# Performance work log

Hardware: AMD Instinct MI355X
Metric: run time of the kernel (lower is better)

## Reference

```python
import jax, jax.numpy as jnp
import numpy as np

COS_EPS = 1e-8  # torch F.cosine_similarity eps


def setup_inputs() -> dict:
    key = jax.random.key(0)
    k1, k2 = jax.random.split(key)
    x = jax.random.normal(k1, (8192, 512), dtype=jnp.float32)
    class_logits = jax.random.normal(k2, (8192, 100), dtype=jnp.float32)
    return {"x": x, "class_logits": class_logits}


def reference(x, class_logits):
    N, D = x.shape
    C = class_logits.shape[1]

    # class_logits.clone().detach()
    logits = jax.lax.stop_gradient(class_logits)
    pred = jax.nn.softmax(logits, axis=1)
    max_logit = pred.max(axis=1)          # [N]
    max_cls = pred.argmax(axis=1)         # [N] int

    # graph(): pairwise cosine similarity = normalize rows + gram matmul
    norms = jnp.linalg.norm(x, axis=1, keepdims=True)
    xn = x / jnp.maximum(norms, COS_EPS)
    mat = xn @ xn.T                       # [N, N]

    x_agg = mat @ x + x                   # [N, D]
    x_new = jax.lax.stop_gradient(x_agg)

    # update_prototype: per-class weighted scatter-add then mean over counts
    weighted = x_new * max_logit[:, None]                     # [N, D]
    sums = jax.ops.segment_sum(weighted, max_cls, num_segments=C)      # [C, D]
    counts = jax.ops.segment_sum(jnp.ones((N,), x.dtype), max_cls, num_segments=C)  # [C]
    prototypes = jnp.where(counts[:, None] > 0,
                           sums / jnp.maximum(counts, 1.0)[:, None],
                           jnp.zeros_like(sums))              # [C, D]

    # inter_class_matrix[i, j] = prototypes[j] - prototypes[i]
    inter_class_matrix = prototypes[None, :, :] - prototypes[:, None, :]  # [C, C, D]
    return prototypes, inter_class_matrix
```

## Files before the change

kernel.cpp:

```cpp
#include <hip/hip_runtime.h>
#include <math.h>

#define N_ROWS 8192
#define D_DIM  512
#define C_CLS  100

typedef unsigned short u16;
typedef unsigned int u32;
typedef __attribute__((ext_vector_type(8))) _Float16 half8;
typedef __attribute__((ext_vector_type(4))) float floatx4;

#define WS_G      0
#define WS_GP     262144
#define WS_INV    5505024
#define WS_WV     5513216
#define WS_CLS    5521408
#define WS_CNT    5529600
#define WS_OFFS   5529728
#define WS_ORDER  5529856
#define WS_U      5538048
#define WS_V      5589248
#define WS_ZTH    5640448

#define LDA 517

typedef const __attribute__((address_space(1))) u32* gp32;
typedef __attribute__((address_space(3))) u32* lp32;
__device__ __forceinline__ void cp16(const u16* g, u16* l) {
    __builtin_amdgcn_global_load_lds((gp32)g, (lp32)l, 16, 0, 0);
}

__device__ __forceinline__ u16 f2h(float v) {
    _Float16 h = (_Float16)v;
    return *(u16*)&h;
}

__global__ __launch_bounds__(256) void kA(const float* __restrict__ logits,
        const float* __restrict__ x, float* __restrict__ wv, int* __restrict__ cls,
        float* __restrict__ inv, u16* __restrict__ zth) {
    __shared__ float xs[16 * LDA];
    __shared__ float ns[4][16];
    __shared__ float sv_s[16];
    int bx = blockIdx.x, t = threadIdx.x;
    if (bx < 1024) {
        int lane = t & 63;
        int row0 = (bx << 3) + ((t >> 6) << 1);
        #pragma unroll
        for (int rr = 0; rr < 2; ++rr) {
            int row = row0 + rr;
            const float* lrow = logits + (size_t)row * C_CLS;
            float v1 = lrow[lane];
            bool has2 = (lane + 64) < C_CLS;
            float v2 = has2 ? lrow[lane + 64] : -INFINITY;
            float m; int idx;
            if (v2 > v1) { m = v2; idx = lane + 64; } else { m = v1; idx = lane; }
            #pragma unroll
            for (int off = 32; off >= 1; off >>= 1) {
                float om = __shfl_down(m, off);
                int   oi = __shfl_down(idx, off);
                if (om > m || (om == m && oi < idx)) { m = om; idx = oi; }
            }
            m = __shfl(m, 0);
            idx = __shfl(idx, 0);
            float s = expf(v1 - m) + (has2 ? expf(v2 - m) : 0.0f);
            #pragma unroll
            for (int off = 32; off >= 1; off >>= 1) s += __shfl_down(s, off);
            if (lane == 0) {
                wv[row] = 1.0f / s;
                cls[row] = idx;
            }
        }
        return;
    }
    int r0 = (bx - 1024) << 4;
    const float* src = x + (size_t)r0 * D_DIM;
    #pragma unroll
    for (int i = 0; i < 8; ++i) {
        int e = i * 1024 + t * 4;
        int r = e >> 9, c = e & 511;
        *(float4*)&xs[r * LDA + c] = *(const float4*)&src[e];
    }
    __syncthreads();
    {
        int r = t & 15, seg = t >> 4;
        const float* row = &xs[r * LDA + seg * 32];
        float ss = 0.f;
        #pragma unroll
        for (int jj = 0; jj < 32; ++jj) { float v = row[jj]; ss += v * v; }
        atomicAdd(&ns[seg & 3][r], 0.f);
        ns[0][r] = 0.f;
        __syncthreads();
        atomicAdd(&ns[0][r], ss);
    }
    __syncthreads();
    if (t < 16) {
        float iv = 1.0f / fmaxf(sqrtf(ns[0][t]), 1e-8f);
        inv[r0 + t] = iv;
        sv_s[t] = sqrtf(iv);
    }
    __syncthreads();
    int c = t >> 1, rq = (t & 1) * 8;
    float svl[8];
    #pragma unroll
    for (int ii = 0; ii < 8; ++ii) svl[ii] = sv_s[rq + ii];
    #pragma unroll
    for (int ct = 0; ct < 4; ++ct) {
        int d = ct * 128 + c;
        u16 o[8];
        #pragma unroll
        for (int ii = 0; ii < 8; ++ii)
            o[ii] = f2h(xs[(rq + ii) * LDA + d] * svl[ii]);
        uint4 val = make_uint4((u32)o[0] | ((u32)o[1] << 16),
                               (u32)o[2] | ((u32)o[3] << 16),
                               (u32)o[4] | ((u32)o[5] << 16),
                               (u32)o[6] | ((u32)o[7] << 16));
        *(uint4*)&zth[(size_t)d * N_ROWS + r0 + rq] = val;
    }
}

__global__ __launch_bounds__(1024) void kB(const int* __restrict__ cls,
        int* __restrict__ cnt, int* __restrict__ offs, int* __restrict__ order) {
    __shared__ int hist[128], scan_s[128], cur[128];
    int t = threadIdx.x;
    if (t < 128) hist[t] = 0;
    __syncthreads();
    for (int m = t; m < N_ROWS; m += 1024) atomicAdd(&hist[cls[m]], 1);
    __syncthreads();
    if (t < 128) scan_s[t] = hist[t];
    __syncthreads();
    #pragma unroll
    for (int d = 1; d < 128; d <<= 1) {
        int add = (t < 128 && t >= d) ? scan_s[t - d] : 0;
        __syncthreads();
        if (t < 128) scan_s[t] += add;
        __syncthreads();
    }
    if (t < 128) {
        int off0 = scan_s[t] - hist[t];
        cur[t] = off0;
        offs[t] = off0;
        cnt[t] = hist[t];
    }
    __syncthreads();
    for (int m = t; m < N_ROWS; m += 1024) {
        int p = atomicAdd(&cur[cls[m]], 1);
        order[p] = m;
    }
}

__global__ __launch_bounds__(256) void kC(const u16* __restrict__ zth,
        const float* __restrict__ x, const float* __restrict__ inv,
        const float* __restrict__ wv, const int* __restrict__ order,
        const int* __restrict__ offs, const int* __restrict__ cnt,
        float* __restrict__ Gp, float* __restrict__ u_arr, float* __restrict__ v_arr) {
    __shared__ __attribute__((aligned(16))) union {
        struct { u16 Ah[2][128 * 32], Bh[2][128 * 32]; } g;
        struct { float us[4][64], vs[4][64]; } uv;
    } sm;
    int bx = blockIdx.x, t = threadIdx.x;
    if (bx >= 320) {
        int idx = bx - 320;
        int c = idx >> 3, jc = idx & 7;
        int g = t >> 6, lane = t & 63;
        int j = jc * 64 + lane;
        int n = cnt[c], o = offs[c];
        float ua = 0.f, va = 0.f;
        for (int p = g; p < n; p += 4) {
            int m = order[o + p];
            float wm = wv[m];
            float wi = wm * inv[m];
            float xv = x[(size_t)m * D_DIM + j];
            ua += wi * xv; va += wm * xv;
        }
        sm.uv.us[g][lane] = ua; sm.uv.vs[g][lane] = va;
        __syncthreads();
        if (g == 0) {
            u_arr[(size_t)c * D_DIM + j] = sm.uv.us[0][lane] + sm.uv.us[1][lane] + sm.uv.us[2][lane] + sm.uv.us[3][lane];
            v_arr[(size_t)c * D_DIM + j] = sm.uv.vs[0][lane] + sm.uv.vs[1][lane] + sm.uv.vs[2][lane] + sm.uv.vs[3][lane];
        }
        return;
    }
    int tile = bx % 10;
    int p = bx / 10;
    int ti = tile < 4 ? 0 : (tile < 7 ? 1 : (tile < 9 ? 2 : 3));
    int tj = tile - (ti == 0 ? 0 : (ti == 1 ? 3 : (ti == 2 ? 5 : 6)));
    int i0 = ti << 7, j0 = tj << 7;
    bool diag = (ti == tj);
    int kb = p << 8;
    int w = t >> 6, l = t & 63;
    int srow = t >> 2, scol = (t & 3) << 3;
    int lm = l & 15, lg = l >> 4;
    floatx4 acc[4][4];
    #pragma unroll
    for (int mi = 0; mi < 4; ++mi)
        #pragma unroll
        for (int ni = 0; ni < 4; ++ni) acc[mi][ni] = (floatx4){0.f, 0.f, 0.f, 0.f};
    int d0 = srow * 32 + scol;
    int d1 = (64 + srow) * 32 + scol;
    const size_t ga0 = (size_t)(i0 + srow) * N_ROWS + kb + scol;
    const size_t ga1 = (size_t)(i0 + 64 + srow) * N_ROWS + kb + scol;
    const size_t gb0 = (size_t)(j0 + srow) * N_ROWS + kb + scol;
    const size_t gb1 = (size_t)(j0 + 64 + srow) * N_ROWS + kb + scol;
    cp16(zth + ga0, sm.g.Ah[0] + d0);
    cp16(zth + ga1, sm.g.Ah[0] + d1);
    if (!diag) {
        cp16(zth + gb0, sm.g.Bh[0] + d0);
        cp16(zth + gb1, sm.g.Bh[0] + d1);
    }
    __syncthreads();
    for (int s = 0; s < 8; ++s) {
        int cur = s & 1, nxt = cur ^ 1;
        if (s + 1 < 8) {
            int ks = (s + 1) << 5;
            cp16(zth + ga0 + ks, sm.g.Ah[nxt] + d0);
            cp16(zth + ga1 + ks, sm.g.Ah[nxt] + d1);
            if (!diag) {
                cp16(zth + gb0 + ks, sm.g.Bh[nxt] + d0);
                cp16(zth + gb1 + ks, sm.g.Bh[nxt] + d1);
            }
        }
        const u16* Bhs = diag ? sm.g.Ah[cur] : sm.g.Bh[cur];
        half8 ah[4], bh[4];
        #pragma unroll
        for (int mi = 0; mi < 4; ++mi) {
            int off = (((w & 1) << 6) + (mi << 4) + lm) * 32 + (lg << 3);
            ah[mi] = *(const half8*)&sm.g.Ah[cur][off];
        }
        #pragma unroll
        for (int ni = 0; ni < 4; ++ni) {
            int off = (((w >> 1) << 6) + (ni << 4) + lm) * 32 + (lg << 3);
            bh[ni] = *(const half8*)&Bhs[off];
        }
        #pragma unroll
        for (int mi = 0; mi < 4; ++mi)
            #pragma unroll
            for (int ni = 0; ni < 4; ++ni)
                acc[mi][ni] = __builtin_amdgcn_mfma_f32_16x16x32_f16(ah[mi], bh[ni], acc[mi][ni], 0, 0, 0);
        __syncthreads();
    }
    float* Gb = Gp + ((size_t)(p * 10 + tile) << 14);
    #pragma unroll
    for (int mi = 0; mi < 4; ++mi) {
        int row0 = ((w & 1) << 6) + (mi << 4) + (lg << 2);
        #pragma unroll
        for (int ni = 0; ni < 4; ++ni) {
            int col = ((w >> 1) << 6) + (ni << 4) + lm;
            #pragma unroll
            for (int r = 0; r < 4; ++r)
                Gb[(size_t)(row0 + r) * 128 + col] = acc[mi][ni][r];
        }
    }
}

__global__ __launch_bounds__(256) void kR(const float* __restrict__ Gp,
                                          float* __restrict__ G) {
    int i = blockIdx.x * 256 + threadIdx.x;
    int r = i >> 9, c = i & 511;
    int tr = r >> 7, tc = c >> 7, rr = r & 127, cc = c & 127;
    if (tr > tc) { int tmp = tr; tr = tc; tc = tmp; tmp = rr; rr = cc; cc = tmp; }
    int tid = tr * 4 + tc - ((tr * (tr + 1)) >> 1);
    const float* src = Gp + ((size_t)tid << 14) + rr * 128 + cc;
    float s = 0.f;
    #pragma unroll
    for (int p = 0; p < 32; ++p) s += src[(size_t)p * 163840];
    G[i] = s;
}

__global__ __launch_bounds__(256) void kD(const float* __restrict__ u_arr,
        const float* __restrict__ v_arr, const int* __restrict__ cnt,
        const float* __restrict__ G, float* __restrict__ out) {
    __shared__ float us[8][512];
    int g = blockIdx.x >> 4;
    int panel = blockIdx.x & 15;
    int t = threadIdx.x;
    for (int idx = t; idx < 8 * 512; idx += 256) {
        int ci = idx >> 9, k = idx & 511;
        int cc = g * 8 + ci;
        us[ci][k] = (cc < C_CLS) ? u_arr[(size_t)cc * D_DIM + k] : 0.f;
    }
    __syncthreads();
    int ci = t >> 5, cj = t & 31;
    int c = g * 8 + ci;
    int j = panel * 32 + cj;
    float acc = 0.f;
    #pragma unroll 8
    for (int k = 0; k < D_DIM; ++k)
        acc += us[ci][k] * G[(size_t)k * D_DIM + j];
    if (c < C_CLS) {
        int n = cnt[c];
        float s = (n > 0) ? 1.0f / (float)n : 0.0f;
        out[(size_t)c * D_DIM + j] = (v_arr[(size_t)c * D_DIM + j] + acc) * s;
    }
}

__global__ __launch_bounds__(256) void kE(const float* __restrict__ proto,
                                          float* __restrict__ inter) {
    int pair = blockIdx.x * 4 + (threadIdx.x >> 6);
    int i = pair / C_CLS;
    int j = pair - i * C_CLS;
    int d = (threadIdx.x & 63) << 3;
    float4 pj0 = *(const float4*)&proto[j * D_DIM + d];
    float4 pj1 = *(const float4*)&proto[j * D_DIM + d + 4];
    float4 pi0 = *(const float4*)&proto[i * D_DIM + d];
    float4 pi1 = *(const float4*)&proto[i * D_DIM + d + 4];
    float4 r0, r1;
    r0.x = pj0.x - pi0.x; r0.y = pj0.y - pi0.y; r0.z = pj0.z - pi0.z; r0.w = pj0.w - pi0.w;
    r1.x = pj1.x - pi1.x; r1.y = pj1.y - pi1.y; r1.z = pj1.z - pi1.z; r1.w = pj1.w - pi1.w;
    *(float4*)&inter[(size_t)pair * D_DIM + d]     = r0;
    *(float4*)&inter[(size_t)pair * D_DIM + d + 4] = r1;
}

extern "C" void kernel_launch(void* const* d_in, const int* in_sizes, int n_in,
                              void* d_out, int out_size, void* d_ws, size_t ws_size,
                              hipStream_t stream) {
    const float* x      = (const float*)d_in[0];
    const float* logits = (const float*)d_in[1];
    float* out = (float*)d_out;
    float* ws  = (float*)d_ws;
    float* G     = ws + WS_G;
    float* Gp    = ws + WS_GP;
    float* inv   = ws + WS_INV;
    float* wv    = ws + WS_WV;
    int*   cls   = (int*)(ws + WS_CLS);
    int*   cnt   = (int*)(ws + WS_CNT);
    int*   offs  = (int*)(ws + WS_OFFS);
    int*   order = (int*)(ws + WS_ORDER);
    float* u_arr = ws + WS_U;
    float* v_arr = ws + WS_V;
    u16* zth = (u16*)(ws + WS_ZTH);

    kA<<<1536, 256, 0, stream>>>(logits, x, wv, cls, inv, zth);
    kB<<<1, 1024, 0, stream>>>(cls, cnt, offs, order);
    kC<<<1120, 256, 0, stream>>>(zth, x, inv, wv, order, offs, cnt, Gp, u_arr, v_arr);
    kR<<<1024, 256, 0, stream>>>(Gp, G);
    kD<<<208, 256, 0, stream>>>(u_arr, v_arr, cnt, G, out);
    kE<<<C_CLS * C_CLS / 4, 256, 0, stream>>>(out, out + C_CLS * D_DIM);
}
```

Before: 168.8 us.

## Replace counting-sort gather with atomic scatter-add and drop sort kernel

Removes the single-block counting-sort kernel that built per-class row orders. The per-class weighted sums u/v and the class counts are now built by having each row atomically add its contributions into its class slot. The accumulators are zeroed by extra blocks appended to the first kernel. This removes a serial launch and the dependency on the sort, but adds many global float atomics that contend on roughly one hundred class rows, and the summation order becomes nondeterministic.

```diff
diff --git a/kernel.cpp b/kernel.cpp
--- a/kernel.cpp
+++ b/kernel.cpp
@@ -16,8 +16,6 @@
 #define WS_WV     5513216
 #define WS_CLS    5521408
 #define WS_CNT    5529600
-#define WS_OFFS   5529728
-#define WS_ORDER  5529856
 #define WS_U      5538048
 #define WS_V      5589248
 #define WS_ZTH    5640448
@@ -37,7 +35,8 @@
 
 __global__ __launch_bounds__(256) void kA(const float* __restrict__ logits,
         const float* __restrict__ x, float* __restrict__ wv, int* __restrict__ cls,
-        float* __restrict__ inv, u16* __restrict__ zth) {
+        float* __restrict__ inv, u16* __restrict__ zth,
+        int* __restrict__ cnt, float* __restrict__ uvz) {
     __shared__ float xs[16 * LDA];
     __shared__ float ns[4][16];
     __shared__ float sv_s[16];
@@ -72,6 +71,21 @@
         }
         return;
     }
+    if (bx >= 1536) {
+        int zid = bx - 1536;
+        if (zid == 0) {
+            if (t < 128) cnt[t] = 0;
+        } else {
+            int gid = (zid - 1) * 256 + t;
+            float4 z = make_float4(0.f, 0.f, 0.f, 0.f);
+            float* p = uvz + (size_t)gid * 16;
+            *(float4*)(p + 0)  = z;
+            *(float4*)(p + 4)  = z;
+            *(float4*)(p + 8)  = z;
+            *(float4*)(p + 12) = z;
+        }
+        return;
+    }
     int r0 = (bx - 1024) << 4;
     const float* src = x + (size_t)r0 * D_DIM;
     #pragma unroll
@@ -87,7 +101,6 @@
         float ss = 0.f;
         #pragma unroll
         for (int jj = 0; jj < 32; ++jj) { float v = row[jj]; ss += v * v; }
-        atomicAdd(&ns[seg & 3][r], 0.f);
         ns[0][r] = 0.f;
         __syncthreads();
         atomicAdd(&ns[0][r], ss);
@@ -118,65 +131,41 @@
     }
 }
 
-__global__ __launch_bounds__(1024) void kB(const int* __restrict__ cls,
-        int* __restrict__ cnt, int* __restrict__ offs, int* __restrict__ order) {
-    __shared__ int hist[128], scan_s[128], cur[128];
-    int t = threadIdx.x;
-    if (t < 128) hist[t] = 0;
-    __syncthreads();
-    for (int m = t; m < N_ROWS; m += 1024) atomicAdd(&hist[cls[m]], 1);
-    __syncthreads();
-    if (t < 128) scan_s[t] = hist[t];
-    __syncthreads();
-    #pragma unroll
-    for (int d = 1; d < 128; d <<= 1) {
-        int add = (t < 128 && t >= d) ? scan_s[t - d] : 0;
-        __syncthreads();
-        if (t < 128) scan_s[t] += add;
-        __syncthreads();
-    }
-    if (t < 128) {
-        int off0 = scan_s[t] - hist[t];
-        cur[t] = off0;
-        offs[t] = off0;
-        cnt[t] = hist[t];
-    }
-    __syncthreads();
-    for (int m = t; m < N_ROWS; m += 1024) {
-        int p = atomicAdd(&cur[cls[m]], 1);
-        order[p] = m;
-    }
-}
-
 __global__ __launch_bounds__(256) void kC(const u16* __restrict__ zth,
         const float* __restrict__ x, const float* __restrict__ inv,
-        const float* __restrict__ wv, const int* __restrict__ order,
-        const int* __restrict__ offs, const int* __restrict__ cnt,
-        float* __restrict__ Gp, float* __restrict__ u_arr, float* __restrict__ v_arr) {
-    __shared__ __attribute__((aligned(16))) union {
-        struct { u16 Ah[2][128 * 32], Bh[2][128 * 32]; } g;
-        struct { float us[4][64], vs[4][64]; } uv;
+        const float* __restrict__ wv, const int* __restrict__ cls,
+        float* __restrict__ Gp, float* __restrict__ u_arr, float* __restrict__ v_arr,
+        int* __restrict__ cnt) {
+    __shared__ __attribute__((aligned(16))) struct {
+        u16 Ah[2][128 * 32], Bh[2][128 * 32];
     } sm;
     int bx = blockIdx.x, t = threadIdx.x;
     if (bx >= 320) {
-        int idx = bx - 320;
-        int c = idx >> 3, jc = idx & 7;
-        int g = t >> 6, lane = t & 63;
-        int j = jc * 64 + lane;
-        int n = cnt[c], o = offs[c];
-        float ua = 0.f, va = 0.f;
-        for (int p = g; p < n; p += 4) {
-            int m = order[o + p];
+        int row0 = (bx - 320) << 5;
+        int w = t >> 6, lane = t & 63;
+        #pragma unroll
+        for (int rr = 0; rr < 8; ++rr) {
+            int m = row0 + w * 8 + rr;
+            int c = cls[m];
             float wm = wv[m];
             float wi = wm * inv[m];
-            float xv = x[(size_t)m * D_DIM + j];
-            ua += wi * xv; va += wm * xv;
-        }
-        sm.uv.us[g][lane] = ua; sm.uv.vs[g][lane] = va;
-        __syncthreads();
-        if (g == 0) {
-            u_arr[(size_t)c * D_DIM + j] = sm.uv.us[0][lane] + sm.uv.us[1][lane] + sm.uv.us[2][lane] + sm.uv.us[3][lane];
-            v_arr[(size_t)c * D_DIM + j] = sm.uv.vs[0][lane] + sm.uv.vs[1][lane] + sm.uv.vs[2][lane] + sm.uv.vs[3][lane];
+            const float4* xr = (const float4*)&x[(size_t)m * D_DIM];
+            float* uc = &u_arr[(size_t)c * D_DIM];
+            float* vc = &v_arr[(size_t)c * D_DIM];
+            #pragma unroll
+            for (int q = 0; q < 2; ++q) {
+                float4 v4 = xr[lane * 2 + q];
+                int base = lane * 8 + q * 4;
+                atomicAdd(&uc[base + 0], wi * v4.x);
+                atomicAdd(&uc[base + 1], wi * v4.y);
+                atomicAdd(&uc[base + 2], wi * v4.z);
+                atomicAdd(&uc[base + 3], wi * v4.w);
+                atomicAdd(&vc[base + 0], wm * v4.x);
+                atomicAdd(&vc[base + 1], wm * v4.y);
+                atomicAdd(&vc[base + 2], wm * v4.z);
+                atomicAdd(&vc[base + 3], wm * v4.w);
+            }
+            if (lane == 0) atomicAdd(&cnt[c], 1);
         }
         return;
     }
@@ -201,30 +190,30 @@
     const size_t ga1 = (size_t)(i0 + 64 + srow) * N_ROWS + kb + scol;
     const size_t gb0 = (size_t)(j0 + srow) * N_ROWS + kb + scol;
     const size_t gb1 = (size_t)(j0 + 64 + srow) * N_ROWS + kb + scol;
-    cp16(zth + ga0, sm.g.Ah[0] + d0);
-    cp16(zth + ga1, sm.g.Ah[0] + d1);
+    cp16(zth + ga0, sm.Ah[0] + d0);
+    cp16(zth + ga1, sm.Ah[0] + d1);
     if (!diag) {
-        cp16(zth + gb0, sm.g.Bh[0] + d0);
-        cp16(zth + gb1, sm.g.Bh[0] + d1);
+        cp16(zth + gb0, sm.Bh[0] + d0);
+        cp16(zth + gb1, sm.Bh[0] + d1);
     }
     __syncthreads();
     for (int s = 0; s < 8; ++s) {
         int cur = s & 1, nxt = cur ^ 1;
         if (s + 1 < 8) {
             int ks = (s + 1) << 5;
-            cp16(zth + ga0 + ks, sm.g.Ah[nxt] + d0);
-            cp16(zth + ga1 + ks, sm.g.Ah[nxt] + d1);
+            cp16(zth + ga0 + ks, sm.Ah[nxt] + d0);
+            cp16(zth + ga1 + ks, sm.Ah[nxt] + d1);
             if (!diag) {
-                cp16(zth + gb0 + ks, sm.g.Bh[nxt] + d0);
-                cp16(zth + gb1 + ks, sm.g.Bh[nxt] + d1);
+                cp16(zth + gb0 + ks, sm.Bh[nxt] + d0);
+                cp16(zth + gb1 + ks, sm.Bh[nxt] + d1);
             }
         }
-        const u16* Bhs = diag ? sm.g.Ah[cur] : sm.g.Bh[cur];
+        const u16* Bhs = diag ? sm.Ah[cur] : sm.Bh[cur];
         half8 ah[4], bh[4];
         #pragma unroll
         for (int mi = 0; mi < 4; ++mi) {
             int off = (((w & 1) << 6) + (mi << 4) + lm) * 32 + (lg << 3);
-            ah[mi] = *(const half8*)&sm.g.Ah[cur][off];
+            ah[mi] = *(const half8*)&sm.Ah[cur][off];
         }
         #pragma unroll
         for (int ni = 0; ni < 4; ++ni) {
@@ -323,15 +312,12 @@
     float* wv    = ws + WS_WV;
     int*   cls   = (int*)(ws + WS_CLS);
     int*   cnt   = (int*)(ws + WS_CNT);
-    int*   offs  = (int*)(ws + WS_OFFS);
-    int*   order = (int*)(ws + WS_ORDER);
     float* u_arr = ws + WS_U;
     float* v_arr = ws + WS_V;
     u16* zth = (u16*)(ws + WS_ZTH);
 
-    kA<<<1536, 256, 0, stream>>>(logits, x, wv, cls, inv, zth);
-    kB<<<1, 1024, 0, stream>>>(cls, cnt, offs, order);
-    kC<<<1120, 256, 0, stream>>>(zth, x, inv, wv, order, offs, cnt, Gp, u_arr, v_arr);
+    kA<<<1562, 256, 0, stream>>>(logits, x, wv, cls, inv, zth, cnt, u_arr);
+    kC<<<576, 256, 0, stream>>>(zth, x, inv, wv, cls, Gp, u_arr, v_arr, cnt);
     kR<<<1024, 256, 0, stream>>>(Gp, G);
     kD<<<208, 256, 0, stream>>>(u_arr, v_arr, cnt, G, out);
     kE<<<C_CLS * C_CLS / 4, 256, 0, stream>>>(out, out + C_CLS * D_DIM);
```

After: 375.1 us. 2.22x slower.
